# Performance work log

Hardware: AMD Instinct MI355X
Metric: run time of the kernel (lower is better)

The kernel has to match this reference:

```python
import jax, jax.numpy as jnp
import numpy as np

B, T, D_IN, D_OUT = 8, 2048, 4096, 4096
N_ADAPTERS, R_MAX = 8, 64


def setup_inputs() -> dict:
    key = jax.random.key(0)
    k_x, k_base, k_idx, k_A, k_B, k_s = jax.random.split(key, 6)
    x = jax.random.normal(k_x, (B, T, D_IN), dtype=jnp.float32)
    base_output = jax.random.normal(k_base, (B, T, D_OUT), dtype=jnp.float32)
    adapter_indices = jax.random.randint(k_idx, (B,), 0, N_ADAPTERS, dtype=jnp.int64)
    # He-uniform init for A (kaiming_uniform with a=sqrt(5) -> bound = 1/sqrt(fan_in))
    bound = 1.0 / np.sqrt(D_IN)
    lora_A = jax.random.uniform(k_A, (N_ADAPTERS, D_IN, R_MAX), dtype=jnp.float32,
                                minval=-bound, maxval=bound)
    # lora_B is zeros at init; use small random values for a non-trivial reference
    lora_B = jax.random.normal(k_B, (N_ADAPTERS, R_MAX, D_OUT), dtype=jnp.float32) * 0.02
    lora_scaling = jax.random.uniform(k_s, (N_ADAPTERS,), dtype=jnp.float32,
                                      minval=0.5, maxval=2.0)
    return {"x": x, "base_output": base_output, "adapter_indices": adapter_indices,
            "lora_A": lora_A, "lora_B": lora_B, "lora_scaling": lora_scaling}


def reference(x, base_output, adapter_indices, lora_A, lora_B, lora_scaling):
    # Gather per-batch adapter weights (adapter index broadcasts over sequence):
    # equivalent to sort-by-adapter -> grouped GEMM -> unsort, since every token
    # in a batch row shares one adapter and all ranks equal r_max.
    A_b = lora_A[adapter_indices]          # [B, D_IN, R]
    B_b = lora_B[adapter_indices]          # [B, R, D_OUT]
    s_b = lora_scaling[adapter_indices]    # [B]
    inter = jnp.einsum('btd,bdr->btr', x, A_b)        # [B, T, R]
    y = jnp.einsum('btr,bro->bto', inter, B_b)        # [B, T, D_OUT]
    return base_output + y * s_b[:, None, None]
```

## Files before the change

kernel.cpp:

```cpp
#include <hip/hip_runtime.h>
#include <hip/hip_bf16.h>
#include <cstdint>
#include <cstddef>

#define BT    16384
#define DIN   4096
#define DOUT  4096
#define RR    64
#define TSEQ  2048
#define NADP  8

typedef float  f32x4  __attribute__((ext_vector_type(4)));
typedef __bf16 bf16x8 __attribute__((ext_vector_type(8)));

static __device__ __forceinline__ unsigned short bf16_bits(float f) {
    return __builtin_bit_cast(unsigned short, (__bf16)f);
}

static __device__ __forceinline__ size_t i2_idx(int mblk, int rb, int mrow, int j) {
    return ((((size_t)mblk * 8 + rb) * 16 + mrow) * 8 + j);
}

__global__ __launch_bounds__(256) void k_prep_a(
    const float* __restrict__ A, __bf16* __restrict__ At2)
{
    const int gtid = blockIdx.x * 256 + threadIdx.x;
    const int r  = gtid & 63;
    const int kb = (gtid >> 6) & (DIN / 8 - 1);
    const int a  = gtid >> 15;
    const float* __restrict__ src = A + (size_t)a * DIN * RR + (size_t)kb * 8 * RR + r;
    unsigned int u[4];
    #pragma unroll
    for (int p = 0; p < 4; ++p) {
        unsigned int lo = bf16_bits(src[(2 * p + 0) * RR]);
        unsigned int hi = bf16_bits(src[(2 * p + 1) * RR]);
        u[p] = lo | (hi << 16);
    }
    *(uint4*)&At2[(size_t)gtid * 8] = make_uint4(u[0], u[1], u[2], u[3]);
}

__global__ __launch_bounds__(256) void k_prep_b(
    const float* __restrict__ Bw, __bf16* __restrict__ Bp)
{
    const int gtid = blockIdx.x * 256 + threadIdx.x;
    const int o  = gtid & (DOUT - 1);
    const int rb = (gtid >> 12) & 7;
    const int a  = gtid >> 15;
    const float* __restrict__ src = Bw + (size_t)a * RR * DOUT + (size_t)rb * 8 * DOUT + o;
    unsigned int u[4];
    #pragma unroll
    for (int p = 0; p < 4; ++p) {
        unsigned int lo = bf16_bits(src[(2 * p + 0) * DOUT]);
        unsigned int hi = bf16_bits(src[(2 * p + 1) * DOUT]);
        u[p] = lo | (hi << 16);
    }
    *(uint4*)&Bp[(size_t)gtid * 8] = make_uint4(u[0], u[1], u[2], u[3]);
}

__global__ __launch_bounds__(256, 1) void k_xa(
    const float* __restrict__ x, const int* __restrict__ idx,
    const __bf16* __restrict__ At2, __bf16* __restrict__ inter2)
{
    const int m0   = blockIdx.x * 64;
    const int a    = idx[m0 / TSEQ];
    const int w    = threadIdx.x >> 6, lane = threadIdx.x & 63;
    const int mr   = lane & 15, kg = lane >> 4;
    const float*  __restrict__ xrow = x + (size_t)(m0 + w * 16 + mr) * DIN + kg * 8;
    const __bf16* __restrict__ Aw = At2 + (size_t)a * RR * DIN + (size_t)(kg * 64 + mr) * 8;

    f32x4 z = {0.f, 0.f, 0.f, 0.f};
    f32x4 acc[4] = {z, z, z, z};

    f32x4  sx0[4], sx1[4];
    bf16x8 sa[4][4];

    #pragma unroll
    for (int s = 0; s < 4; ++s) {
        sx0[s] = *(const f32x4*)(xrow + s * 32);
        sx1[s] = *(const f32x4*)(xrow + s * 32 + 4);
        #pragma unroll
        for (int n = 0; n < 4; ++n)
            sa[s][n] = *(const bf16x8*)(Aw + ((size_t)s * 256 + n * 16) * 8);
    }

    #pragma unroll 4
    for (int ks = 0; ks < 124; ++ks) {
        const int s = ks & 3;
        f32x4 u0 = sx0[s], u1 = sx1[s];
        bf16x8 a0 = sa[s][0], a1 = sa[s][1], a2 = sa[s][2], a3 = sa[s][3];
        sx0[s] = *(const f32x4*)(xrow + (ks + 4) * 32);
        sx1[s] = *(const f32x4*)(xrow + (ks + 4) * 32 + 4);
        #pragma unroll
        for (int n = 0; n < 4; ++n)
            sa[s][n] = *(const bf16x8*)(Aw + ((size_t)(ks + 4) * 256 + n * 16) * 8);
        bf16x8 af;
        af[0] = (__bf16)u0[0]; af[1] = (__bf16)u0[1];
        af[2] = (__bf16)u0[2]; af[3] = (__bf16)u0[3];
        af[4] = (__bf16)u1[0]; af[5] = (__bf16)u1[1];
        af[6] = (__bf16)u1[2]; af[7] = (__bf16)u1[3];
        acc[0] = __builtin_amdgcn_mfma_f32_16x16x32_bf16(af, a0, acc[0], 0, 0, 0);
        acc[1] = __builtin_amdgcn_mfma_f32_16x16x32_bf16(af, a1, acc[1], 0, 0, 0);
        acc[2] = __builtin_amdgcn_mfma_f32_16x16x32_bf16(af, a2, acc[2], 0, 0, 0);
        acc[3] = __builtin_amdgcn_mfma_f32_16x16x32_bf16(af, a3, acc[3], 0, 0, 0);
    }

    #pragma unroll
    for (int ks = 124; ks < 128; ++ks) {
        const int s = ks & 3;
        f32x4 u0 = sx0[s], u1 = sx1[s];
        bf16x8 af;
        af[0] = (__bf16)u0[0]; af[1] = (__bf16)u0[1];
        af[2] = (__bf16)u0[2]; af[3] = (__bf16)u0[3];
        af[4] = (__bf16)u1[0]; af[5] = (__bf16)u1[1];
        af[6] = (__bf16)u1[2]; af[7] = (__bf16)u1[3];
        #pragma unroll
        for (int n = 0; n < 4; ++n)
            acc[n] = __builtin_amdgcn_mfma_f32_16x16x32_bf16(af, sa[s][n], acc[n], 0, 0, 0);
    }

    const int mblk = blockIdx.x * 4 + w;
    #pragma unroll
    for (int n = 0; n < 4; ++n) {
        const int rb = n * 2 + (mr >> 3), j = mr & 7;
        #pragma unroll
        for (int q = 0; q < 4; ++q)
            inter2[i2_idx(mblk, rb, kg * 4 + q, j)] = (__bf16)acc[n][q];
    }
}

__global__ __launch_bounds__(256) void k_by(
    const __bf16* __restrict__ inter2, const float* __restrict__ base,
    const int* __restrict__ idx, const __bf16* __restrict__ Bp,
    const float* __restrict__ scal, float* __restrict__ out)
{
    const int o0 = blockIdx.x * 64;
    const int m0 = blockIdx.y * 64;
    const int a  = idx[m0 / TSEQ];
    const float s = scal[a];
    const __bf16* __restrict__ Ba = Bp + (size_t)a * RR * DOUT;
    const int lane = threadIdx.x & 63;
    const int w    = threadIdx.x >> 6;
    const int mr   = lane & 15, kg = lane >> 4;
    const int oc   = o0 + w * 16 + mr;

    f32x4 z = {0.f, 0.f, 0.f, 0.f};
    f32x4 acc[4] = {z, z, z, z};

    #pragma unroll
    for (int ksub = 0; ksub < 2; ++ksub) {
        const int rb = ksub * 4 + kg;
        bf16x8 bfA = *(const bf16x8*)&Ba[((size_t)rb * DOUT + oc) * 8];
        #pragma unroll
        for (int mt = 0; mt < 4; ++mt) {
            bf16x8 afB = *(const bf16x8*)&inter2[i2_idx(m0 / 16 + mt, rb, mr, 0)];
            acc[mt] = __builtin_amdgcn_mfma_f32_16x16x32_bf16(bfA, afB, acc[mt], 0, 0, 0);
        }
    }

    #pragma unroll
    for (int mt = 0; mt < 4; ++mt) {
        size_t off = (size_t)(m0 + mt * 16 + mr) * DOUT + o0 + w * 16 + kg * 4;
        float4 bv = *(const float4*)&base[off];
        float4 o;
        o.x = bv.x + s * acc[mt][0];
        o.y = bv.y + s * acc[mt][1];
        o.z = bv.z + s * acc[mt][2];
        o.w = bv.w + s * acc[mt][3];
        *(float4*)&out[off] = o;
    }
}

__global__ __launch_bounds__(256) void k_xa_fb(
    const float* __restrict__ x, const int* __restrict__ idx,
    const float* __restrict__ A, __bf16* __restrict__ inter)
{
    const int m0   = blockIdx.x * 32;
    const int a    = idx[m0 / TSEQ];
    const float* __restrict__ Aa = A + (size_t)a * DIN * RR;
    const int lane = threadIdx.x & 63;
    const int rw   = threadIdx.x >> 6;
    const int mr   = lane & 15, kg = lane >> 4;
    const int rcol = rw * 16 + mr;
    const float* __restrict__ xrow0 = x + (size_t)(m0 + mr) * DIN;
    const float* __restrict__ xrow1 = x + (size_t)(m0 + 16 + mr) * DIN;

    f32x4 acc0 = {0.f, 0.f, 0.f, 0.f};
    f32x4 acc1 = {0.f, 0.f, 0.f, 0.f};

    for (int k0 = 0; k0 < DIN; k0 += 64) {
        #pragma unroll
        for (int ksub = 0; ksub < 2; ++ksub) {
            const int koff = k0 + ksub * 32 + kg * 8;
            float4 u0 = *(const float4*)&xrow0[koff];
            float4 u1 = *(const float4*)&xrow0[koff + 4];
            float4 v0 = *(const float4*)&xrow1[koff];
            float4 v1 = *(const float4*)&xrow1[koff + 4];
            bf16x8 af0, af1;
            af0[0] = (__bf16)u0.x; af0[1] = (__bf16)u0.y;
            af0[2] = (__bf16)u0.z; af0[3] = (__bf16)u0.w;
            af0[4] = (__bf16)u1.x; af0[5] = (__bf16)u1.y;
            af0[6] = (__bf16)u1.z; af0[7] = (__bf16)u1.w;
            af1[0] = (__bf16)v0.x; af1[1] = (__bf16)v0.y;
            af1[2] = (__bf16)v0.z; af1[3] = (__bf16)v0.w;
            af1[4] = (__bf16)v1.x; af1[5] = (__bf16)v1.y;
            af1[6] = (__bf16)v1.z; af1[7] = (__bf16)v1.w;
            const float* ap = &Aa[(size_t)koff * RR + rcol];
            bf16x8 bf;
            bf[0] = (__bf16)ap[0 * RR]; bf[1] = (__bf16)ap[1 * RR];
            bf[2] = (__bf16)ap[2 * RR]; bf[3] = (__bf16)ap[3 * RR];
            bf[4] = (__bf16)ap[4 * RR]; bf[5] = (__bf16)ap[5 * RR];
            bf[6] = (__bf16)ap[6 * RR]; bf[7] = (__bf16)ap[7 * RR];
            acc0 = __builtin_amdgcn_mfma_f32_16x16x32_bf16(af0, bf, acc0, 0, 0, 0);
            acc1 = __builtin_amdgcn_mfma_f32_16x16x32_bf16(af1, bf, acc1, 0, 0, 0);
        }
    }
    #pragma unroll
    for (int q = 0; q < 4; ++q) {
        inter[(size_t)(m0 + kg * 4 + q) * RR + rcol]      = (__bf16)acc0[q];
        inter[(size_t)(m0 + 16 + kg * 4 + q) * RR + rcol] = (__bf16)acc1[q];
    }
}

__global__ __launch_bounds__(256) void k_by_fb(
    const __bf16* __restrict__ inter, const float* __restrict__ base,
    const int* __restrict__ idx, const float* __restrict__ Bw,
    const float* __restrict__ scal, float* __restrict__ out)
{
    const int o0 = blockIdx.x * 64;
    const int m0 = blockIdx.y * 64;
    const int a  = idx[m0 / TSEQ];
    const float s = scal[a];
    const float* __restrict__ Ba = Bw + (size_t)a * RR * DOUT;
    const int lane = threadIdx.x & 63;
    const int w    = threadIdx.x >> 6;
    const int mr   = lane & 15, kg = lane >> 4;
    const int oc   = o0 + w * 16 + mr;

    f32x4 z = {0.f, 0.f, 0.f, 0.f};
    f32x4 acc[4] = {z, z, z, z};

    #pragma unroll
    for (int ksub = 0; ksub < 2; ++ksub) {
        const int kb = ksub * 32 + kg * 8;
        const float* bp = &Ba[(size_t)kb * DOUT + oc];
        bf16x8 bf;
        bf[0] = (__bf16)bp[0 * DOUT]; bf[1] = (__bf16)bp[1 * DOUT];
        bf[2] = (__bf16)bp[2 * DOUT]; bf[3] = (__bf16)bp[3 * DOUT];
        bf[4] = (__bf16)bp[4 * DOUT]; bf[5] = (__bf16)bp[5 * DOUT];
        bf[6] = (__bf16)bp[6 * DOUT]; bf[7] = (__bf16)bp[7 * DOUT];
        #pragma unroll
        for (int mt = 0; mt < 4; ++mt) {
            bf16x8 af = *(const bf16x8*)&inter[(size_t)(m0 + mt * 16 + mr) * RR + kb];
            acc[mt] = __builtin_amdgcn_mfma_f32_16x16x32_bf16(af, bf, acc[mt], 0, 0, 0);
        }
    }
    #pragma unroll
    for (int mt = 0; mt < 4; ++mt) {
        #pragma unroll
        for (int q = 0; q < 4; ++q) {
            size_t off = (size_t)(m0 + mt * 16 + kg * 4 + q) * DOUT + oc;
            out[off] = base[off] + s * acc[mt][q];
        }
    }
}

extern "C" void kernel_launch(void* const* d_in, const int* in_sizes, int n_in,
                              void* d_out, int out_size, void* d_ws, size_t ws_size,
                              hipStream_t stream)
{
    const float* x    = (const float*)d_in[0];
    const float* base = (const float*)d_in[1];
    const int*   idx  = (const int*)  d_in[2];
    const float* A    = (const float*)d_in[3];
    const float* Bw   = (const float*)d_in[4];
    const float* scal = (const float*)d_in[5];
    float* out = (float*)d_out;

    const size_t INTER_B = (size_t)BT * RR * 2;
    const size_t AT_B    = (size_t)NADP * RR * DIN * 2;
    const size_t BT_B    = (size_t)NADP * DOUT * RR * 2;

    if (ws_size >= INTER_B + AT_B + BT_B) {
        __bf16* inter2 = (__bf16*)d_ws;
        __bf16* At2    = (__bf16*)((char*)d_ws + INTER_B);
        __bf16* Bp     = (__bf16*)((char*)d_ws + INTER_B + AT_B);
        k_prep_a<<<dim3(1024), 256, 0, stream>>>(A, At2);
        k_prep_b<<<dim3(1024), 256, 0, stream>>>(Bw, Bp);
        k_xa<<<dim3(BT / 64),            256, 0, stream>>>(x, idx, At2, inter2);
        k_by<<<dim3(DOUT / 64, BT / 64), 256, 0, stream>>>(inter2, base, idx, Bp, scal, out);
    } else {
        __bf16* inter = (__bf16*)d_ws;
        k_xa_fb<<<dim3(BT / 32),            256, 0, stream>>>(x, idx, A, inter);
        k_by_fb<<<dim3(DOUT / 64, BT / 64), 256, 0, stream>>>(inter, base, idx, Bw, scal, out);
    }
}
```

Measured before the change: 205.0 us.

## Split x@A reduction over K into two halves and sum partials in B-GEMM

```diff
diff --git a/kernel.cpp b/kernel.cpp
--- a/kernel.cpp
+++ b/kernel.cpp
@@ -57,6 +57,130 @@
     *(uint4*)&Bp[(size_t)gtid * 8] = make_uint4(u[0], u[1], u[2], u[3]);
 }
 
+__global__ __launch_bounds__(256, 2) void k_xa_half(
+    const float* __restrict__ x, const int* __restrict__ idx,
+    const __bf16* __restrict__ At2,
+    __bf16* __restrict__ part0, __bf16* __restrict__ part1)
+{
+    const int m0   = blockIdx.x * 64;
+    const int h    = blockIdx.y;
+    const int a    = idx[m0 / TSEQ];
+    const int w    = threadIdx.x >> 6, lane = threadIdx.x & 63;
+    const int mr   = lane & 15, kg = lane >> 4;
+    const int koff0 = h * 2048;
+    __bf16* __restrict__ dst = h ? part1 : part0;
+
+    const float* __restrict__ xrow =
+        x + (size_t)(m0 + w * 16 + mr) * DIN + koff0 + kg * 8;
+    const __bf16* __restrict__ Aw =
+        At2 + (size_t)a * RR * DIN + (size_t)koff0 * 64 + (size_t)(kg * 64 + mr) * 8;
+
+    f32x4 z = {0.f, 0.f, 0.f, 0.f};
+    f32x4 acc[4] = {z, z, z, z};
+
+    f32x4  sx0[4], sx1[4];
+    bf16x8 sa[4][4];
+
+    #pragma unroll
+    for (int s = 0; s < 4; ++s) {
+        sx0[s] = *(const f32x4*)(xrow + s * 32);
+        sx1[s] = *(const f32x4*)(xrow + s * 32 + 4);
+        #pragma unroll
+        for (int n = 0; n < 4; ++n)
+            sa[s][n] = *(const bf16x8*)(Aw + ((size_t)s * 256 + n * 16) * 8);
+    }
+
+    #pragma unroll 4
+    for (int ks = 0; ks < 60; ++ks) {
+        const int s = ks & 3;
+        f32x4 u0 = sx0[s], u1 = sx1[s];
+        bf16x8 a0 = sa[s][0], a1 = sa[s][1], a2 = sa[s][2], a3 = sa[s][3];
+        sx0[s] = *(const f32x4*)(xrow + (ks + 4) * 32);
+        sx1[s] = *(const f32x4*)(xrow + (ks + 4) * 32 + 4);
+        #pragma unroll
+        for (int n = 0; n < 4; ++n)
+            sa[s][n] = *(const bf16x8*)(Aw + ((size_t)(ks + 4) * 256 + n * 16) * 8);
+        bf16x8 af;
+        af[0] = (__bf16)u0[0]; af[1] = (__bf16)u0[1];
+        af[2] = (__bf16)u0[2]; af[3] = (__bf16)u0[3];
+        af[4] = (__bf16)u1[0]; af[5] = (__bf16)u1[1];
+        af[6] = (__bf16)u1[2]; af[7] = (__bf16)u1[3];
+        acc[0] = __builtin_amdgcn_mfma_f32_16x16x32_bf16(af, a0, acc[0], 0, 0, 0);
+        acc[1] = __builtin_amdgcn_mfma_f32_16x16x32_bf16(af, a1, acc[1], 0, 0, 0);
+        acc[2] = __builtin_amdgcn_mfma_f32_16x16x32_bf16(af, a2, acc[2], 0, 0, 0);
+        acc[3] = __builtin_amdgcn_mfma_f32_16x16x32_bf16(af, a3, acc[3], 0, 0, 0);
+    }
+
+    #pragma unroll
+    for (int ks = 60; ks < 64; ++ks) {
+        const int s = ks & 3;
+        f32x4 u0 = sx0[s], u1 = sx1[s];
+        bf16x8 af;
+        af[0] = (__bf16)u0[0]; af[1] = (__bf16)u0[1];
+        af[2] = (__bf16)u0[2]; af[3] = (__bf16)u0[3];
+        af[4] = (__bf16)u1[0]; af[5] = (__bf16)u1[1];
+        af[6] = (__bf16)u1[2]; af[7] = (__bf16)u1[3];
+        #pragma unroll
+        for (int n = 0; n < 4; ++n)
+            acc[n] = __builtin_amdgcn_mfma_f32_16x16x32_bf16(af, sa[s][n], acc[n], 0, 0, 0);
+    }
+
+    const int mblk = blockIdx.x * 4 + w;
+    #pragma unroll
+    for (int n = 0; n < 4; ++n) {
+        const int rb = n * 2 + (mr >> 3), j = mr & 7;
+        #pragma unroll
+        for (int q = 0; q < 4; ++q)
+            dst[i2_idx(mblk, rb, kg * 4 + q, j)] = (__bf16)acc[n][q];
+    }
+}
+
+__global__ __launch_bounds__(256) void k_by2(
+    const __bf16* __restrict__ part0, const __bf16* __restrict__ part1,
+    const float* __restrict__ base, const int* __restrict__ idx,
+    const __bf16* __restrict__ Bp, const float* __restrict__ scal,
+    float* __restrict__ out)
+{
+    const int o0 = blockIdx.x * 64;
+    const int m0 = blockIdx.y * 64;
+    const int a  = idx[m0 / TSEQ];
+    const float s = scal[a];
+    const __bf16* __restrict__ Ba = Bp + (size_t)a * RR * DOUT;
+    const int lane = threadIdx.x & 63;
+    const int w    = threadIdx.x >> 6;
+    const int mr   = lane & 15, kg = lane >> 4;
+    const int oc   = o0 + w * 16 + mr;
+
+    f32x4 z = {0.f, 0.f, 0.f, 0.f};
+    f32x4 acc[4] = {z, z, z, z};
+
+    #pragma unroll
+    for (int ksub = 0; ksub < 2; ++ksub) {
+        const int rb = ksub * 4 + kg;
+        bf16x8 bfA = *(const bf16x8*)&Ba[((size_t)rb * DOUT + oc) * 8];
+        #pragma unroll
+        for (int mt = 0; mt < 4; ++mt) {
+            const size_t ii = i2_idx(m0 / 16 + mt, rb, mr, 0);
+            bf16x8 af0 = *(const bf16x8*)&part0[ii];
+            bf16x8 af1 = *(const bf16x8*)&part1[ii];
+            acc[mt] = __builtin_amdgcn_mfma_f32_16x16x32_bf16(bfA, af0, acc[mt], 0, 0, 0);
+            acc[mt] = __builtin_amdgcn_mfma_f32_16x16x32_bf16(bfA, af1, acc[mt], 0, 0, 0);
+        }
+    }
+
+    #pragma unroll
+    for (int mt = 0; mt < 4; ++mt) {
+        size_t off = (size_t)(m0 + mt * 16 + mr) * DOUT + o0 + w * 16 + kg * 4;
+        float4 bv = *(const float4*)&base[off];
+        float4 o;
+        o.x = bv.x + s * acc[mt][0];
+        o.y = bv.y + s * acc[mt][1];
+        o.z = bv.z + s * acc[mt][2];
+        o.w = bv.w + s * acc[mt][3];
+        *(float4*)&out[off] = o;
+    }
+}
+
 __global__ __launch_bounds__(256, 1) void k_xa(
     const float* __restrict__ x, const int* __restrict__ idx,
     const __bf16* __restrict__ At2, __bf16* __restrict__ inter2)
@@ -70,7 +194,6 @@
 
     f32x4 z = {0.f, 0.f, 0.f, 0.f};
     f32x4 acc[4] = {z, z, z, z};
-
     f32x4  sx0[4], sx1[4];
     bf16x8 sa[4][4];
 
@@ -280,7 +403,16 @@
     const size_t AT_B    = (size_t)NADP * RR * DIN * 2;
     const size_t BT_B    = (size_t)NADP * DOUT * RR * 2;
 
-    if (ws_size >= INTER_B + AT_B + BT_B) {
+    if (ws_size >= 2 * INTER_B + AT_B + BT_B) {
+        __bf16* part0 = (__bf16*)d_ws;
+        __bf16* part1 = (__bf16*)((char*)d_ws + INTER_B);
+        __bf16* At2   = (__bf16*)((char*)d_ws + 2 * INTER_B);
+        __bf16* Bp    = (__bf16*)((char*)d_ws + 2 * INTER_B + AT_B);
+        k_prep_a<<<dim3(1024), 256, 0, stream>>>(A, At2);
+        k_prep_b<<<dim3(1024), 256, 0, stream>>>(Bw, Bp);
+        k_xa_half<<<dim3(BT / 64, 2),      256, 0, stream>>>(x, idx, At2, part0, part1);
+        k_by2<<<dim3(DOUT / 64, BT / 64),  256, 0, stream>>>(part0, part1, base, idx, Bp, scal, out);
+    } else if (ws_size >= INTER_B + AT_B + BT_B) {
         __bf16* inter2 = (__bf16*)d_ws;
         __bf16* At2    = (__bf16*)((char*)d_ws + INTER_B);
         __bf16* Bp     = (__bf16*)((char*)d_ws + INTER_B + AT_B);
```

After: 216.6 us. 5.6% more time.

## Split the x·A reduction over K chunks with a separate partial-sum reduce kernel

Applied to the files above, without the earlier changes.

```diff
diff --git a/kernel.cpp b/kernel.cpp
--- a/kernel.cpp
+++ b/kernel.cpp
@@ -9,6 +9,8 @@
 #define RR    64
 #define TSEQ  2048
 #define NADP  8
+#define NCH   16
+#define KCH   (DIN / NCH)
 
 typedef float  f32x4  __attribute__((ext_vector_type(4)));
 typedef __bf16 bf16x8 __attribute__((ext_vector_type(8)));
@@ -19,6 +21,13 @@
 
 static __device__ __forceinline__ size_t i2_idx(int mblk, int rb, int mrow, int j) {
     return ((((size_t)mblk * 8 + rb) * 16 + mrow) * 8 + j);
+}
+
+static __device__ __forceinline__ bf16x8 cvt8(float4 a, float4 b) {
+    bf16x8 v;
+    v[0] = (__bf16)a.x; v[1] = (__bf16)a.y; v[2] = (__bf16)a.z; v[3] = (__bf16)a.w;
+    v[4] = (__bf16)b.x; v[5] = (__bf16)b.y; v[6] = (__bf16)b.z; v[7] = (__bf16)b.w;
+    return v;
 }
 
 __global__ __launch_bounds__(256) void k_prep_a(
@@ -57,75 +66,59 @@
     *(uint4*)&Bp[(size_t)gtid * 8] = make_uint4(u[0], u[1], u[2], u[3]);
 }
 
-__global__ __launch_bounds__(256, 1) void k_xa(
+__global__ __launch_bounds__(256) void k_xa_split(
     const float* __restrict__ x, const int* __restrict__ idx,
-    const __bf16* __restrict__ At2, __bf16* __restrict__ inter2)
-{
-    const int m0   = blockIdx.x * 64;
+    const __bf16* __restrict__ At2, __bf16* __restrict__ parts)
+{
+    const int mb   = blockIdx.x;
+    const int kc   = blockIdx.y;
+    const int m0   = mb * 16;
     const int a    = idx[m0 / TSEQ];
-    const int w    = threadIdx.x >> 6, lane = threadIdx.x & 63;
-    const int mr   = lane & 15, kg = lane >> 4;
-    const float*  __restrict__ xrow = x + (size_t)(m0 + w * 16 + mr) * DIN + kg * 8;
-    const __bf16* __restrict__ Aw = At2 + (size_t)a * RR * DIN + (size_t)(kg * 64 + mr) * 8;
-
-    f32x4 z = {0.f, 0.f, 0.f, 0.f};
-    f32x4 acc[4] = {z, z, z, z};
-
-    f32x4  sx0[4], sx1[4];
-    bf16x8 sa[4][4];
-
-    #pragma unroll
-    for (int s = 0; s < 4; ++s) {
-        sx0[s] = *(const f32x4*)(xrow + s * 32);
-        sx1[s] = *(const f32x4*)(xrow + s * 32 + 4);
-        #pragma unroll
-        for (int n = 0; n < 4; ++n)
-            sa[s][n] = *(const bf16x8*)(Aw + ((size_t)s * 256 + n * 16) * 8);
-    }
-
-    #pragma unroll 4
-    for (int ks = 0; ks < 124; ++ks) {
-        const int s = ks & 3;
-        f32x4 u0 = sx0[s], u1 = sx1[s];
-        bf16x8 a0 = sa[s][0], a1 = sa[s][1], a2 = sa[s][2], a3 = sa[s][3];
-        sx0[s] = *(const f32x4*)(xrow + (ks + 4) * 32);
-        sx1[s] = *(const f32x4*)(xrow + (ks + 4) * 32 + 4);
-        #pragma unroll
-        for (int n = 0; n < 4; ++n)
-            sa[s][n] = *(const bf16x8*)(Aw + ((size_t)(ks + 4) * 256 + n * 16) * 8);
-        bf16x8 af;
-        af[0] = (__bf16)u0[0]; af[1] = (__bf16)u0[1];
-        af[2] = (__bf16)u0[2]; af[3] = (__bf16)u0[3];
-        af[4] = (__bf16)u1[0]; af[5] = (__bf16)u1[1];
-        af[6] = (__bf16)u1[2]; af[7] = (__bf16)u1[3];
-        acc[0] = __builtin_amdgcn_mfma_f32_16x16x32_bf16(af, a0, acc[0], 0, 0, 0);
-        acc[1] = __builtin_amdgcn_mfma_f32_16x16x32_bf16(af, a1, acc[1], 0, 0, 0);
-        acc[2] = __builtin_amdgcn_mfma_f32_16x16x32_bf16(af, a2, acc[2], 0, 0, 0);
-        acc[3] = __builtin_amdgcn_mfma_f32_16x16x32_bf16(af, a3, acc[3], 0, 0, 0);
-    }
-
-    #pragma unroll
-    for (int ks = 124; ks < 128; ++ks) {
-        const int s = ks & 3;
-        f32x4 u0 = sx0[s], u1 = sx1[s];
-        bf16x8 af;
-        af[0] = (__bf16)u0[0]; af[1] = (__bf16)u0[1];
-        af[2] = (__bf16)u0[2]; af[3] = (__bf16)u0[3];
-        af[4] = (__bf16)u1[0]; af[5] = (__bf16)u1[1];
-        af[6] = (__bf16)u1[2]; af[7] = (__bf16)u1[3];
-        #pragma unroll
-        for (int n = 0; n < 4; ++n)
-            acc[n] = __builtin_amdgcn_mfma_f32_16x16x32_bf16(af, sa[s][n], acc[n], 0, 0, 0);
-    }
-
-    const int mblk = blockIdx.x * 4 + w;
-    #pragma unroll
-    for (int n = 0; n < 4; ++n) {
-        const int rb = n * 2 + (mr >> 3), j = mr & 7;
-        #pragma unroll
-        for (int q = 0; q < 4; ++q)
-            inter2[i2_idx(mblk, rb, kg * 4 + q, j)] = (__bf16)acc[n][q];
-    }
+    const int rw   = threadIdx.x >> 6, lane = threadIdx.x & 63;
+    const int mr   = lane & 15, kg = lane >> 4;
+    const int rcol = rw * 16 + mr;
+
+    const float*  __restrict__ xrow = x + (size_t)(m0 + mr) * DIN + kc * KCH + kg * 8;
+    const __bf16* __restrict__ Aw   = At2 + (size_t)a * RR * DIN;
+    const int kqb = kc * (KCH / 8);
+
+    f32x4 acc = {0.f, 0.f, 0.f, 0.f};
+
+    #pragma unroll
+    for (int step = 0; step < 8; ++step) {
+        float4 u0 = *(const float4*)(xrow + step * 32);
+        float4 u1 = *(const float4*)(xrow + step * 32 + 4);
+        bf16x8 bfw = *(const bf16x8*)&Aw[((size_t)(kqb + step * 4 + kg) * 64 + rcol) * 8];
+        acc = __builtin_amdgcn_mfma_f32_16x16x32_bf16(cvt8(u0, u1), bfw, acc, 0, 0, 0);
+    }
+
+    __bf16* __restrict__ part = parts + (size_t)kc * (BT / 16) * 1024;
+    const int rb = rw * 2 + (mr >> 3), j = mr & 7;
+    #pragma unroll
+    for (int q = 0; q < 4; ++q)
+        part[i2_idx(mb, rb, kg * 4 + q, j)] = (__bf16)acc[q];
+}
+
+__global__ __launch_bounds__(256) void k_reduce(
+    const __bf16* __restrict__ parts, __bf16* __restrict__ inter2)
+{
+    const int t = blockIdx.x * 256 + threadIdx.x;
+    const size_t off = (size_t)t * 8;
+    float s[8] = {};
+    #pragma unroll
+    for (int c = 0; c < NCH; ++c) {
+        bf16x8 v = *(const bf16x8*)&parts[(size_t)c * (BT / 16) * 1024 + off];
+        #pragma unroll
+        for (int e = 0; e < 8; ++e) s[e] += (float)v[e];
+    }
+    unsigned int u[4];
+    #pragma unroll
+    for (int p = 0; p < 4; ++p) {
+        unsigned int lo = bf16_bits(s[2 * p + 0]);
+        unsigned int hi = bf16_bits(s[2 * p + 1]);
+        u[p] = lo | (hi << 16);
+    }
+    *(uint4*)&inter2[off] = make_uint4(u[0], u[1], u[2], u[3]);
 }
 
 __global__ __launch_bounds__(256) void k_by(
@@ -170,6 +163,66 @@
     }
 }
 
+__global__ __launch_bounds__(256, 1) void k_xa(
+    const float* __restrict__ x, const int* __restrict__ idx,
+    const __bf16* __restrict__ At2, __bf16* __restrict__ inter2)
+{
+    const int m0   = blockIdx.x * 64;
+    const int a    = idx[m0 / TSEQ];
+    const int w    = threadIdx.x >> 6, lane = threadIdx.x & 63;
+    const int mr   = lane & 15, kg = lane >> 4;
+    const float*  __restrict__ xrow = x + (size_t)(m0 + w * 16 + mr) * DIN + kg * 8;
+    const __bf16* __restrict__ Aw = At2 + (size_t)a * RR * DIN + (size_t)(kg * 64 + mr) * 8;
+
+    f32x4 z = {0.f, 0.f, 0.f, 0.f};
+    f32x4 acc[4] = {z, z, z, z};
+    float4 sx0[4], sx1[4];
+    bf16x8 sa[4][4];
+
+    #pragma unroll
+    for (int s = 0; s < 4; ++s) {
+        sx0[s] = *(const float4*)(xrow + s * 32);
+        sx1[s] = *(const float4*)(xrow + s * 32 + 4);
+        #pragma unroll
+        for (int n = 0; n < 4; ++n)
+            sa[s][n] = *(const bf16x8*)(Aw + ((size_t)s * 256 + n * 16) * 8);
+    }
+
+    #pragma unroll 4
+    for (int ks = 0; ks < 124; ++ks) {
+        const int s = ks & 3;
+        float4 u0 = sx0[s], u1 = sx1[s];
+        bf16x8 a0 = sa[s][0], a1 = sa[s][1], a2 = sa[s][2], a3 = sa[s][3];
+        sx0[s] = *(const float4*)(xrow + (ks + 4) * 32);
+        sx1[s] = *(const float4*)(xrow + (ks + 4) * 32 + 4);
+        #pragma unroll
+        for (int n = 0; n < 4; ++n)
+            sa[s][n] = *(const bf16x8*)(Aw + ((size_t)(ks + 4) * 256 + n * 16) * 8);
+        bf16x8 af = cvt8(u0, u1);
+        acc[0] = __builtin_amdgcn_mfma_f32_16x16x32_bf16(af, a0, acc[0], 0, 0, 0);
+        acc[1] = __builtin_amdgcn_mfma_f32_16x16x32_bf16(af, a1, acc[1], 0, 0, 0);
+        acc[2] = __builtin_amdgcn_mfma_f32_16x16x32_bf16(af, a2, acc[2], 0, 0, 0);
+        acc[3] = __builtin_amdgcn_mfma_f32_16x16x32_bf16(af, a3, acc[3], 0, 0, 0);
+    }
+    #pragma unroll
+    for (int ks = 124; ks < 128; ++ks) {
+        const int s = ks & 3;
+        bf16x8 af = cvt8(sx0[s], sx1[s]);
+        #pragma unroll
+        for (int n = 0; n < 4; ++n)
+            acc[n] = __builtin_amdgcn_mfma_f32_16x16x32_bf16(af, sa[s][n], acc[n], 0, 0, 0);
+    }
+
+    const int mblk = blockIdx.x * 4 + w;
+    #pragma unroll
+    for (int n = 0; n < 4; ++n) {
+        const int rb = n * 2 + (mr >> 3), j = mr & 7;
+        #pragma unroll
+        for (int q = 0; q < 4; ++q)
+            inter2[i2_idx(mblk, rb, kg * 4 + q, j)] = (__bf16)acc[n][q];
+    }
+}
+
 __global__ __launch_bounds__(256) void k_xa_fb(
     const float* __restrict__ x, const int* __restrict__ idx,
     const float* __restrict__ A, __bf16* __restrict__ inter)
@@ -195,15 +248,8 @@
             float4 u1 = *(const float4*)&xrow0[koff + 4];
             float4 v0 = *(const float4*)&xrow1[koff];
             float4 v1 = *(const float4*)&xrow1[koff + 4];
-            bf16x8 af0, af1;
-            af0[0] = (__bf16)u0.x; af0[1] = (__bf16)u0.y;
-            af0[2] = (__bf16)u0.z; af0[3] = (__bf16)u0.w;
-            af0[4] = (__bf16)u1.x; af0[5] = (__bf16)u1.y;
-            af0[6] = (__bf16)u1.z; af0[7] = (__bf16)u1.w;
-            af1[0] = (__bf16)v0.x; af1[1] = (__bf16)v0.y;
-            af1[2] = (__bf16)v0.z; af1[3] = (__bf16)v0.w;
-            af1[4] = (__bf16)v1.x; af1[5] = (__bf16)v1.y;
-            af1[6] = (__bf16)v1.z; af1[7] = (__bf16)v1.w;
+            bf16x8 af0 = cvt8(u0, u1);
+            bf16x8 af1 = cvt8(v0, v1);
             const float* ap = &Aa[(size_t)koff * RR + rcol];
             bf16x8 bf;
             bf[0] = (__bf16)ap[0 * RR]; bf[1] = (__bf16)ap[1 * RR];
@@ -279,8 +325,19 @@
     const size_t INTER_B = (size_t)BT * RR * 2;
     const size_t AT_B    = (size_t)NADP * RR * DIN * 2;
     const size_t BT_B    = (size_t)NADP * DOUT * RR * 2;
-
-    if (ws_size >= INTER_B + AT_B + BT_B) {
+    const size_t PART_B  = (size_t)NCH * INTER_B;
+
+    if (ws_size >= INTER_B + AT_B + BT_B + PART_B) {
+        __bf16* inter2 = (__bf16*)d_ws;
+        __bf16* At2    = (__bf16*)((char*)d_ws + INTER_B);
+        __bf16* Bp     = (__bf16*)((char*)d_ws + INTER_B + AT_B);
+        __bf16* parts  = (__bf16*)((char*)d_ws + INTER_B + AT_B + BT_B);
+        k_prep_a<<<dim3(1024), 256, 0, stream>>>(A, At2);
+        k_prep_b<<<dim3(1024), 256, 0, stream>>>(Bw, Bp);
+        k_xa_split<<<dim3(BT / 16, NCH), 256, 0, stream>>>(x, idx, At2, parts);
+        k_reduce<<<dim3(512),            256, 0, stream>>>(parts, inter2);
+        k_by<<<dim3(DOUT / 64, BT / 64), 256, 0, stream>>>(inter2, base, idx, Bp, scal, out);
+    } else if (ws_size >= INTER_B + AT_B + BT_B) {
         __bf16* inter2 = (__bf16*)d_ws;
         __bf16* At2    = (__bf16*)((char*)d_ws + INTER_B);
         __bf16* Bp     = (__bf16*)((char*)d_ws + INTER_B + AT_B);
```

Result: slower. 271.8 us (+32.6%).
